# Performance work log

Measured on AMD Instinct MI355X. Metric: run time of the kernel, lower is better.

## Reference

```python
import jax, jax.numpy as jnp
import numpy as np

B = 65536
NUM_INPUTS = 128
H0, H1 = 512, 512
K = 200
MIN_W = 0.001
MIN_H = 0.001
MIN_D = 0.001
EDGE_CONST = float(np.log(np.exp(1.0 - 0.001) - 1.0))  # in-place edge derivative value
LN_EPS = 1e-5


def setup_inputs() -> dict:
    key = jax.random.key(0)
    ks = jax.random.split(key, 10)
    f32 = jnp.float32
    inputs = jax.random.normal(ks[0], (B, NUM_INPUTS), dtype=f32)
    W1 = jax.random.normal(ks[1], (H0, NUM_INPUTS), dtype=f32) / np.sqrt(NUM_INPUTS)
    b1 = jnp.zeros((H0,), f32)
    g1 = jnp.ones((H0,), f32)
    be1 = jnp.zeros((H0,), f32)
    W2 = jax.random.normal(ks[2], (H1, H0), dtype=f32) / np.sqrt(H0)
    b2 = jnp.zeros((H1,), f32)
    g2 = jnp.ones((H1,), f32)
    be2 = jnp.zeros((H1,), f32)
    WV = jax.random.normal(ks[3], (3 * K - 1, H1), dtype=f32) / np.sqrt(H1)
    bV = jnp.zeros((3 * K - 1,), f32)
    Wa = jax.random.normal(ks[4], (1, H1), dtype=f32) / np.sqrt(H1)
    ba = jnp.zeros((1,), f32)
    Wb = jax.random.normal(ks[5], (1, H1), dtype=f32) / np.sqrt(H1)
    bb = jnp.zeros((1,), f32)
    return {"inputs": inputs, "W1": W1, "b1": b1, "g1": g1, "be1": be1,
            "W2": W2, "b2": b2, "g2": g2, "be2": be2,
            "WV": WV, "bV": bV, "Wa": Wa, "ba": ba, "Wb": Wb, "bb": bb}


def _layernorm(x, g, b):
    m = jnp.mean(x, axis=-1, keepdims=True)
    v = jnp.mean(jnp.square(x - m), axis=-1, keepdims=True)
    return (x - m) * jax.lax.rsqrt(v + LN_EPS) * g + b


def _spline_forward(inputs, W1, b1, g1, be1, W2, b2, g2, be2, WV, bV, Wa, ba, Wb, bb):
    x = jax.nn.relu(_layernorm(inputs @ W1.T + b1, g1, be1))
    x = jax.nn.relu(_layernorm(x @ W2.T + b2, g2, be2))
    sp = x @ WV.T + bV                      # [B, 3K-1]
    scale_a = jnp.exp(x @ Wa.T + ba)        # [B, 1]
    scale_b = x @ Wb.T + bb                 # [B, 1]

    Wp = jax.nn.softmax(sp[:, :K], axis=1)
    Hp = jax.nn.softmax(sp[:, K:2 * K], axis=1)
    Dp = sp[:, 2 * K:]                      # [B, K-1]
    Wp = MIN_W + (1.0 - MIN_W * K) * Wp
    Hp = MIN_H + (1.0 - MIN_H * K) * Hp
    Dp = MIN_D + jax.nn.softplus(Dp)
    bsz = inputs.shape[0]
    edge = jnp.full((bsz, 1), EDGE_CONST, dtype=inputs.dtype)
    D = jnp.concatenate([edge, Dp, edge], axis=-1)          # [B, K+1]

    zero = jnp.zeros((bsz, 1), dtype=inputs.dtype)
    cw = jnp.concatenate([zero, jnp.cumsum(Wp, axis=-1)], axis=-1)
    cw = cw.at[:, -1].set(1.0)                              # [B, K+1]
    widths = cw[:, 1:] - cw[:, :-1]                         # [B, K]
    ch = jnp.concatenate([zero, jnp.cumsum(Hp, axis=-1)], axis=-1)
    ch = scale_a * ch + scale_b                             # [B, K+1]
    heights = ch[:, 1:] - ch[:, :-1]                        # [B, K]

    tau = ((jnp.arange(K, dtype=inputs.dtype) + 0.5) / K)   # [K]
    tau = jnp.broadcast_to(tau, (bsz, K))

    # sum(tau >= bins) - 1 == searchsorted(bins, tau, side='right') - 1
    bin_idx = jax.vmap(lambda b, t: jnp.searchsorted(b, t, side='right'))(cw, tau) - 1

    ta = lambda a: jnp.take_along_axis(a, bin_idx, axis=-1)
    in_cw = ta(cw)
    in_w = ta(widths)
    in_ch = ta(ch)
    in_h = ta(heights)
    in_delta = ta(heights / widths)
    d0 = ta(D)
    d1 = ta(D[:, 1:])

    theta = (tau - in_cw) / in_w
    t1mt = theta * (1.0 - theta)
    numer = in_h * (in_delta * jnp.square(theta) + d0 * t1mt)
    denom = in_delta + (d0 + d1 - 2.0 * in_delta) * t1mt
    return in_ch + numer / denom            # [B, K]


def reference(inputs, W1, b1, g1, be1, W2, b2, g2, be2, WV, bV, Wa, ba, Wb, bb):
    return _spline_forward(inputs, W1, b1, g1, be1, W2, b2, g2, be2, WV, bV, Wa, ba, Wb, bb)
```

## Files before the change

kernel.cpp:

```cpp
#include <hip/hip_runtime.h>
#include <stdint.h>

typedef __bf16 bf16;
typedef __bf16 bf16x8 __attribute__((ext_vector_type(8)));
typedef __bf16 bf16x4 __attribute__((ext_vector_type(4)));
typedef float  f32x4  __attribute__((ext_vector_type(4)));
typedef uint32_t u32;

#define BATCH    65536
#define NCAT     640
#define SPSTRIDE 604

__device__ __forceinline__ void async16(const void* g, void* l) {
    __builtin_amdgcn_global_load_lds(
        (const u32 __attribute__((address_space(1)))*)g,
        (u32 __attribute__((address_space(3)))*)l,
        16, 0, 0);
}

__global__ __launch_bounds__(256) void prep_kernel(
    const float* W1, const float* W2, const float* WV,
    const float* bV, const float* Wa, const float* ba,
    const float* Wb, const float* bb,
    bf16* w1b, bf16* w2b, bf16* wcat, float* bcat)
{
    int idx = blockIdx.x * 256 + threadIdx.x;
    const int n1 = 512 * 128, n2 = 512 * 512, n3 = NCAT * 512;
    if (idx < n1) { w1b[idx] = (bf16)W1[idx]; return; }
    idx -= n1;
    if (idx < n2) { w2b[idx] = (bf16)W2[idx]; return; }
    idx -= n2;
    if (idx < n3) {
        int n = idx >> 9, k = idx & 511;
        float v = 0.f;
        if (n < 599)       v = WV[n * 512 + k];
        else if (n == 599) v = Wa[k];
        else if (n == 600) v = Wb[k];
        wcat[idx] = (bf16)v;
        return;
    }
    idx -= n3;
    if (idx < NCAT) {
        float v = 0.f;
        if (idx < 599)       v = bV[idx];
        else if (idx == 599) v = ba[0];
        else if (idx == 600) v = bb[0];
        bcat[idx] = v;
    }
}

template <int KDIM, bool AF32>
__global__ __launch_bounds__(512, 4) void gemm_ln(
    const void* Av, const bf16* __restrict__ W,
    const float* __restrict__ bias, const float* __restrict__ gamma,
    const float* __restrict__ beta, bf16* out)
{
    constexpr int ABUF = AF32 ? 8192 : 4096;
    __shared__ __align__(16) char smem[2 * ABUF + 65536];
    char* Abase = smem;
    char* Bbase = smem + 2 * ABUF;

    const int t = threadIdx.x;
    const int lane = t & 63, wid = t >> 6;
    const int wm = wid >> 2, wn = wid & 3;
    const int l16 = lane & 15, g16 = lane >> 4;
    const long row0 = (long)blockIdx.x * 64;

    constexpr int NT = KDIM / 32;

    f32x4 acc[2][8];
#pragma unroll
    for (int a = 0; a < 2; ++a)
#pragma unroll
        for (int b = 0; b < 8; ++b) acc[a][b] = (f32x4){0.f, 0.f, 0.f, 0.f};

    auto stageA = [&](int kt, int bi) {
        const int k0 = kt * 32;
        if (AF32) {
            int row = wid * 8 + (lane >> 3);
            int colf = ((lane & 7) * 4) ^ (((lane >> 3) & 7) << 2);
            const float* src = (const float*)Av + (row0 + row) * KDIM + k0 + colf;
            async16(src, Abase + bi * ABUF + wid * 1024);
        } else {
            if (wid < 4) {
                int row = wid * 16 + (lane >> 2);
                const bf16* src = (const bf16*)Av + (row0 + row) * (long)KDIM + k0 + (lane & 3) * 8;
                async16(src, Abase + bi * ABUF + wid * 1024);
            }
        }
    };
    auto stageB = [&](int kt, int bi) {
        const int k0 = kt * 32;
#pragma unroll
        for (int c = 0; c < 4; ++c) {
            int call = wid * 4 + c;
            int row = call * 16 + (lane >> 2);
            const bf16* src = W + (long)row * KDIM + k0 + (lane & 3) * 8;
            async16(src, Bbase + bi * 32768 + call * 1024);
        }
    };

    stageA(0, 0); stageB(0, 0);
    __syncthreads();

    for (int kt = 0; kt < NT; ++kt) {
        const int bi = kt & 1;
        if (kt + 1 < NT) { stageA(kt + 1, bi ^ 1); stageB(kt + 1, bi ^ 1); }

        bf16x8 af[2];
        if (AF32) {
            const float* Af = (const float*)(Abase + bi * ABUF);
#pragma unroll
            for (int fm = 0; fm < 2; ++fm) {
                int r = wm * 32 + fm * 16 + l16;
                int m8 = (r & 7) << 2;
                f32x4 v0 = *(const f32x4*)(Af + r * 32 + ((g16 * 8)     ^ m8));
                f32x4 v1 = *(const f32x4*)(Af + r * 32 + ((g16 * 8 + 4) ^ m8));
                bf16x8 h;
                h[0]=(bf16)v0[0]; h[1]=(bf16)v0[1]; h[2]=(bf16)v0[2]; h[3]=(bf16)v0[3];
                h[4]=(bf16)v1[0]; h[5]=(bf16)v1[1]; h[6]=(bf16)v1[2]; h[7]=(bf16)v1[3];
                af[fm] = h;
            }
        } else {
            const bf16* Ab = (const bf16*)(Abase + bi * ABUF);
#pragma unroll
            for (int fm = 0; fm < 2; ++fm)
                af[fm] = *(const bf16x8*)(Ab + (wm * 32 + fm * 16 + l16) * 32 + g16 * 8);
        }
        const bf16* Bb = (const bf16*)(Bbase + bi * 32768);
#pragma unroll
        for (int fn = 0; fn < 8; ++fn) {
            bf16x8 bv = *(const bf16x8*)(Bb + (wn * 128 + fn * 16 + l16) * 32 + g16 * 8);
            acc[0][fn] = __builtin_amdgcn_mfma_f32_16x16x32_bf16(af[0], bv, acc[0][fn], 0, 0, 0);
            acc[1][fn] = __builtin_amdgcn_mfma_f32_16x16x32_bf16(af[1], bv, acc[1][fn], 0, 0, 0);
        }
        __syncthreads();
    }

    float* Psum = (float*)Abase;
    float* Psq  = (float*)(Abase + 1024);
#pragma unroll
    for (int fm = 0; fm < 2; ++fm)
#pragma unroll
        for (int fn = 0; fn < 8; ++fn) {
            float bv = bias[wn * 128 + fn * 16 + l16];
#pragma unroll
            for (int i = 0; i < 4; ++i) acc[fm][fn][i] += bv;
        }
#pragma unroll
    for (int fm = 0; fm < 2; ++fm)
#pragma unroll
        for (int i = 0; i < 4; ++i) {
            float s = 0.f, q = 0.f;
#pragma unroll
            for (int fn = 0; fn < 8; ++fn) { float v = acc[fm][fn][i]; s += v; q += v * v; }
#pragma unroll
            for (int m = 1; m < 16; m <<= 1) { s += __shfl_xor(s, m); q += __shfl_xor(q, m); }
            if (l16 == 0) {
                int lr = wm * 32 + fm * 16 + g16 * 4 + i;
                Psum[lr * 4 + wn] = s; Psq[lr * 4 + wn] = q;
            }
        }
    __syncthreads();
#pragma unroll
    for (int fm = 0; fm < 2; ++fm)
#pragma unroll
        for (int i = 0; i < 4; ++i) {
            int lr = wm * 32 + fm * 16 + g16 * 4 + i;
            float s = Psum[lr * 4 + 0] + Psum[lr * 4 + 1] + Psum[lr * 4 + 2] + Psum[lr * 4 + 3];
            float q = Psq[lr * 4 + 0] + Psq[lr * 4 + 1] + Psq[lr * 4 + 2] + Psq[lr * 4 + 3];
            float mean = s * (1.f / 512.f);
            float var  = q * (1.f / 512.f) - mean * mean;
            float rstd = rsqrtf(var + 1e-5f);
            long grow = row0 + lr;
#pragma unroll
            for (int fn = 0; fn < 8; ++fn) {
                int col = wn * 128 + fn * 16 + l16;
                float o = (acc[fm][fn][i] - mean) * rstd * gamma[col] + beta[col];
                out[grow * 512 + col] = (bf16)fmaxf(o, 0.f);
            }
        }
}

__global__ __launch_bounds__(512, 2) void gemm_cat(
    const bf16* __restrict__ A, const bf16* __restrict__ W,
    const float* __restrict__ bcat, bf16* __restrict__ sp, float* __restrict__ ab)
{
    __shared__ __align__(16) char smem[16384 + 81920];
    char* Abase = smem;
    char* Bbase = smem + 16384;

    const int t = threadIdx.x;
    const int lane = t & 63, wid = t >> 6;
    const int wm = wid >> 2, wn = wid & 3;
    const int l16 = lane & 15, g16 = lane >> 4;
    const long row0 = (long)blockIdx.x * 128;

    f32x4 acc[4][10];
#pragma unroll
    for (int a = 0; a < 4; ++a)
#pragma unroll
        for (int b = 0; b < 10; ++b) acc[a][b] = (f32x4){0.f, 0.f, 0.f, 0.f};

    auto stageA = [&](int kt, int bi) {
        int row = wid * 16 + (lane >> 2);
        const bf16* src = A + (row0 + row) * 512 + kt * 32 + (lane & 3) * 8;
        async16(src, Abase + bi * 8192 + wid * 1024);
    };
    auto stageB = [&](int kt, int bi) {
#pragma unroll
        for (int c = 0; c < 5; ++c) {
            int call = wid * 5 + c;
            int row = call * 16 + (lane >> 2);
            const bf16* src = W + (long)row * 512 + kt * 32 + (lane & 3) * 8;
            async16(src, Bbase + bi * 40960 + call * 1024);
        }
    };

    stageA(0, 0); stageB(0, 0);
    __syncthreads();

    for (int kt = 0; kt < 16; ++kt) {
        const int bi = kt & 1;
        if (kt < 15) { stageA(kt + 1, bi ^ 1); stageB(kt + 1, bi ^ 1); }
        const bf16* Ab = (const bf16*)(Abase + bi * 8192);
        const bf16* Bb = (const bf16*)(Bbase + bi * 40960);
        bf16x8 af[4];
#pragma unroll
        for (int fm = 0; fm < 4; ++fm)
            af[fm] = *(const bf16x8*)(Ab + (wm * 64 + fm * 16 + l16) * 32 + g16 * 8);
#pragma unroll
        for (int fn = 0; fn < 10; ++fn) {
            bf16x8 bv = *(const bf16x8*)(Bb + (wn * 160 + fn * 16 + l16) * 32 + g16 * 8);
#pragma unroll
            for (int fm = 0; fm < 4; ++fm)
                acc[fm][fn] = __builtin_amdgcn_mfma_f32_16x16x32_bf16(af[fm], bv, acc[fm][fn], 0, 0, 0);
        }
        __syncthreads();
    }

#pragma unroll
    for (int fn = 0; fn < 10; ++fn) {
        int col = wn * 160 + fn * 16 + l16;
        float bv = (col <= 600) ? bcat[col] : 0.f;
#pragma unroll
        for (int fm = 0; fm < 4; ++fm)
#pragma unroll
            for (int i = 0; i < 4; ++i) {
                long grow = row0 + wm * 64 + fm * 16 + g16 * 4 + i;
                float v = acc[fm][fn][i] + bv;
                if (col < 599)       sp[grow * SPSTRIDE + col] = (bf16)v;
                else if (col == 599) ab[grow * 2 + 0] = v;
                else if (col == 600) ab[grow * 2 + 1] = v;
            }
    }
}

__global__ __launch_bounds__(256) void spline_kernel(
    const bf16* __restrict__ sp, const float* __restrict__ ab, float* __restrict__ out)
{
    const int t = threadIdx.x;
    const int lane = t & 63, wid = t >> 6;
    const long row = (long)blockIdx.x * 4 + wid;
    const bf16* spr = sp + row * SPSTRIDE;
    const bool act = lane < 50;
    const float EC = 0.53974247f;

    const float sa = __expf(ab[row * 2 + 0]);
    const float sb = ab[row * 2 + 1];

    auto rng = [](float x) -> int {
        int v = (int)ceilf(fmaf(200.f, x, -0.5f));
        return v < 0 ? 0 : (v > 200 ? 200 : v);
    };

    float p0, p1, p2, p3;
    {
        float x0, x1, x2v, x3;
        if (act) {
            bf16x4 v = *(const bf16x4*)&spr[4 * lane];
            x0 = (float)v[0]; x1 = (float)v[1]; x2v = (float)v[2]; x3 = (float)v[3];
        } else { x0 = x1 = x2v = x3 = -1e30f; }
        float m = fmaxf(fmaxf(x0, x1), fmaxf(x2v, x3));
#pragma unroll
        for (int d = 1; d < 64; d <<= 1) m = fmaxf(m, __shfl_xor(m, d));
        float e0 = act ? __expf(x0 - m) : 0.f;
        float e1 = act ? __expf(x1 - m) : 0.f;
        float e2 = act ? __expf(x2v - m) : 0.f;
        float e3 = act ? __expf(x3 - m) : 0.f;
        float s = e0 + e1 + e2 + e3;
#pragma unroll
        for (int d = 1; d < 64; d <<= 1) s += __shfl_xor(s, d);
        float inv = 0.8f / s;
        p0 = act ? fmaf(e0, inv, 0.001f) : 0.f;
        p1 = act ? fmaf(e1, inv, 0.001f) : 0.f;
        p2 = act ? fmaf(e2, inv, 0.001f) : 0.f;
        p3 = act ? fmaf(e3, inv, 0.001f) : 0.f;
    }
    float c0 = p0, c1 = c0 + p1, c2 = c1 + p2, c3 = c2 + p3;
    float run = c3, ts = run;
#pragma unroll
    for (int d = 1; d < 64; d <<= 1) { float u = __shfl_up(ts, d); if (lane >= d) ts += u; }
    float excl  = ts - run;
    float nexcl = __shfl_down(excl, 1);
    float cwl0 = excl, cwl1 = excl + c0, cwl2 = excl + c1, cwl3 = excl + c2;
    float cwr3 = (lane == 49) ? 1.0f : nexcl;

    float hp0, hp1, hp2, hp3;
    {
        float x0, x1, x2v, x3;
        if (act) {
            bf16x4 v = *(const bf16x4*)&spr[200 + 4 * lane];
            x0 = (float)v[0]; x1 = (float)v[1]; x2v = (float)v[2]; x3 = (float)v[3];
        } else { x0 = x1 = x2v = x3 = -1e30f; }
        float m = fmaxf(fmaxf(x0, x1), fmaxf(x2v, x3));
#pragma unroll
        for (int d = 1; d < 64; d <<= 1) m = fmaxf(m, __shfl_xor(m, d));
        float e0 = act ? __expf(x0 - m) : 0.f;
        float e1 = act ? __expf(x1 - m) : 0.f;
        float e2 = act ? __expf(x2v - m) : 0.f;
        float e3 = act ? __expf(x3 - m) : 0.f;
        float s = e0 + e1 + e2 + e3;
#pragma unroll
        for (int d = 1; d < 64; d <<= 1) s += __shfl_xor(s, d);
        float inv = 0.8f / s;
        hp0 = act ? fmaf(e0, inv, 0.001f) : 0.f;
        hp1 = act ? fmaf(e1, inv, 0.001f) : 0.f;
        hp2 = act ? fmaf(e2, inv, 0.001f) : 0.f;
        hp3 = act ? fmaf(e3, inv, 0.001f) : 0.f;
    }
    float hc0 = hp0, hc1 = hc0 + hp1, hc2 = hc1 + hp2, hc3 = hc2 + hp3;
    float hrun = hc3, hts = hrun;
#pragma unroll
    for (int d = 1; d < 64; d <<= 1) { float u = __shfl_up(hts, d); if (lane >= d) hts += u; }
    float hexcl  = hts - hrun;
    float nhexcl = __shfl_down(hexcl, 1);
    float ch0 = fmaf(sa, hexcl, sb);
    float ch1 = fmaf(sa, hexcl + hc0, sb);
    float ch2 = fmaf(sa, hexcl + hc1, sb);
    float ch3 = fmaf(sa, hexcl + hc2, sb);
    float chr3 = fmaf(sa, nhexcl, sb);

    float dv0, dv1, dv2, dv3;
    {
        float x0 = 0.f, x1 = 0.f, x2v = 0.f, x3 = 0.f;
        if (act) {
            bf16x4 v = *(const bf16x4*)&spr[400 + 4 * lane];
            x0 = (float)v[0]; x1 = (float)v[1]; x2v = (float)v[2]; x3 = (float)v[3];
        }
        auto spls = [](float x) {
            return fmaxf(x, 0.f) + __logf(1.f + __expf(-fabsf(x))) + 0.001f;
        };
        dv0 = spls(x0); dv1 = spls(x1); dv2 = spls(x2v); dv3 = spls(x3);
    }
    if (lane == 49) dv3 = EC;
    float dprev = __shfl_up(dv3, 1);
    if (lane == 0) dprev = EC;

    int b0 = rng(cwl0), b1 = rng(cwl1), b2 = rng(cwl2), b3 = rng(cwl3);
    int b4 = (lane == 49) ? 200 : rng(nexcl);

    if (act) {
        float* orow = out + (size_t)row * 200;
        auto emit = [&](int lo, int hi, float wl, float wr_, float hl, float hr,
                        float d0, float d1) {
            float w = wr_ - wl;
            float h = hr - hl;
            float invw = 1.f / w;
            float delta = h * invw;
            float dd2 = d0 + d1 - 2.f * delta;
            for (int jj = lo; jj < hi; ++jj) {
                float tau = ((float)jj + 0.5f) * (1.f / 200.f);
                float th = (tau - wl) * invw;
                float t1 = th * (1.f - th);
                float numer = h * (delta * th * th + d0 * t1);
                float denom = fmaf(dd2, t1, delta);
                orow[jj] = hl + numer / denom;
            }
        };
        emit(b0, b1, cwl0, cwl1, ch0, ch1, dprev, dv0);
        emit(b1, b2, cwl1, cwl2, ch1, ch2, dv0,   dv1);
        emit(b2, b3, cwl2, cwl3, ch2, ch3, dv1,   dv2);
        emit(b3, b4, cwl3, cwr3, ch3, chr3, dv2,  dv3);
    }
}

extern "C" void kernel_launch(void* const* d_in, const int* in_sizes, int n_in,
                              void* d_out, int out_size, void* d_ws, size_t ws_size,
                              hipStream_t stream)
{
    const float* inputs = (const float*)d_in[0];
    const float* W1  = (const float*)d_in[1];
    const float* b1  = (const float*)d_in[2];
    const float* g1  = (const float*)d_in[3];
    const float* be1 = (const float*)d_in[4];
    const float* W2  = (const float*)d_in[5];
    const float* b2  = (const float*)d_in[6];
    const float* g2  = (const float*)d_in[7];
    const float* be2 = (const float*)d_in[8];
    const float* WV  = (const float*)d_in[9];
    const float* bV  = (const float*)d_in[10];
    const float* Wa  = (const float*)d_in[11];
    const float* ba  = (const float*)d_in[12];
    const float* Wb  = (const float*)d_in[13];
    const float* bb  = (const float*)d_in[14];
    float* out = (float*)d_out;

    char* ws = (char*)d_ws;
    bf16*  w1b  = (bf16*) (ws + 0);
    bf16*  w2b  = (bf16*) (ws + 131072);
    bf16*  wcat = (bf16*) (ws + 655360);
    float* bcat = (float*)(ws + 1310720);
    float* ab   = (float*)(ws + 1313280);
    bf16*  x    = (bf16*) (ws + 2097152);
    bf16*  spb  = (bf16*) (ws + 69206016);

    const int preptot = 512 * 128 + 512 * 512 + NCAT * 512 + NCAT;
    prep_kernel<<<(preptot + 255) / 256, 256, 0, stream>>>(
        W1, W2, WV, bV, Wa, ba, Wb, bb, w1b, w2b, wcat, bcat);

    gemm_ln<128, true ><<<BATCH / 64, 512, 0, stream>>>(inputs, w1b, b1, g1, be1, x);
    gemm_ln<512, false><<<BATCH / 64, 512, 0, stream>>>(x,      w2b, b2, g2, be2, x);
    gemm_cat<<<BATCH / 128, 512, 0, stream>>>(x, wcat, bcat, spb, ab);
    spline_kernel<<<BATCH / 4, 256, 0, stream>>>(spb, ab, out);
}
```

Before: 263.5 us.

## Pre-convert inputs to bf16, split gemm_cat along N, use LDS-indexed spline evaluation

Three separate changes. The prep kernel now converts the fp32 inputs to bf16 up front, so the first GEMM loads bf16 A tiles instead of converting fp32 in LDS. gemm_cat splits its N dimension across two blocks, halving per-block LDS and accumulators so that four blocks can be resident per CU. The spline kernel writes per-row knot tables and a bin index per output into LDS, then has each lane evaluate outputs j = lane + 50k, giving coalesced stores and balanced work instead of variable-length per-lane loops. The extra conversion pass costs one more read and write of the input, and the split GEMM reads the A tile twice.

```diff
diff --git a/kernel.cpp b/kernel.cpp
--- a/kernel.cpp
+++ b/kernel.cpp
@@ -21,11 +21,22 @@
 __global__ __launch_bounds__(256) void prep_kernel(
     const float* W1, const float* W2, const float* WV,
     const float* bV, const float* Wa, const float* ba,
-    const float* Wb, const float* bb,
-    bf16* w1b, bf16* w2b, bf16* wcat, float* bcat)
+    const float* Wb, const float* bb, const float* inputs,
+    bf16* w1b, bf16* w2b, bf16* wcat, float* bcat, bf16* xin)
 {
     int idx = blockIdx.x * 256 + threadIdx.x;
     const int n1 = 512 * 128, n2 = 512 * 512, n3 = NCAT * 512;
+    const int n5 = BATCH * 128 / 8;
+    if (idx < n5) {
+        const float4* src = (const float4*)(inputs + idx * 8);
+        float4 v0 = src[0], v1 = src[1];
+        bf16x8 h;
+        h[0]=(bf16)v0.x; h[1]=(bf16)v0.y; h[2]=(bf16)v0.z; h[3]=(bf16)v0.w;
+        h[4]=(bf16)v1.x; h[5]=(bf16)v1.y; h[6]=(bf16)v1.z; h[7]=(bf16)v1.w;
+        *(bf16x8*)&xin[idx * 8] = h;
+        return;
+    }
+    idx -= n5;
     if (idx < n1) { w1b[idx] = (bf16)W1[idx]; return; }
     idx -= n1;
     if (idx < n2) { w2b[idx] = (bf16)W2[idx]; return; }
@@ -49,23 +60,21 @@
     }
 }
 
-template <int KDIM, bool AF32>
+template <int KDIM>
 __global__ __launch_bounds__(512, 4) void gemm_ln(
-    const void* Av, const bf16* __restrict__ W,
+    const bf16* __restrict__ A, const bf16* __restrict__ W,
     const float* __restrict__ bias, const float* __restrict__ gamma,
     const float* __restrict__ beta, bf16* out)
 {
-    constexpr int ABUF = AF32 ? 8192 : 4096;
-    __shared__ __align__(16) char smem[2 * ABUF + 65536];
+    __shared__ __align__(16) char smem[8192 + 65536];
     char* Abase = smem;
-    char* Bbase = smem + 2 * ABUF;
+    char* Bbase = smem + 8192;
 
     const int t = threadIdx.x;
     const int lane = t & 63, wid = t >> 6;
     const int wm = wid >> 2, wn = wid & 3;
     const int l16 = lane & 15, g16 = lane >> 4;
     const long row0 = (long)blockIdx.x * 64;
-
     constexpr int NT = KDIM / 32;
 
     f32x4 acc[2][8];
@@ -75,27 +84,18 @@
         for (int b = 0; b < 8; ++b) acc[a][b] = (f32x4){0.f, 0.f, 0.f, 0.f};
 
     auto stageA = [&](int kt, int bi) {
-        const int k0 = kt * 32;
-        if (AF32) {
-            int row = wid * 8 + (lane >> 3);
-            int colf = ((lane & 7) * 4) ^ (((lane >> 3) & 7) << 2);
-            const float* src = (const float*)Av + (row0 + row) * KDIM + k0 + colf;
-            async16(src, Abase + bi * ABUF + wid * 1024);
-        } else {
-            if (wid < 4) {
-                int row = wid * 16 + (lane >> 2);
-                const bf16* src = (const bf16*)Av + (row0 + row) * (long)KDIM + k0 + (lane & 3) * 8;
-                async16(src, Abase + bi * ABUF + wid * 1024);
-            }
+        if (wid < 4) {
+            int row = wid * 16 + (lane >> 2);
+            const bf16* src = A + (row0 + row) * (long)KDIM + kt * 32 + (lane & 3) * 8;
+            async16(src, Abase + bi * 4096 + wid * 1024);
         }
     };
     auto stageB = [&](int kt, int bi) {
-        const int k0 = kt * 32;
 #pragma unroll
         for (int c = 0; c < 4; ++c) {
             int call = wid * 4 + c;
             int row = call * 16 + (lane >> 2);
-            const bf16* src = W + (long)row * KDIM + k0 + (lane & 3) * 8;
+            const bf16* src = W + (long)row * KDIM + kt * 32 + (lane & 3) * 8;
             async16(src, Bbase + bi * 32768 + call * 1024);
         }
     };
@@ -106,28 +106,12 @@
     for (int kt = 0; kt < NT; ++kt) {
         const int bi = kt & 1;
         if (kt + 1 < NT) { stageA(kt + 1, bi ^ 1); stageB(kt + 1, bi ^ 1); }
-
+        const bf16* Ab = (const bf16*)(Abase + bi * 4096);
+        const bf16* Bb = (const bf16*)(Bbase + bi * 32768);
         bf16x8 af[2];
-        if (AF32) {
-            const float* Af = (const float*)(Abase + bi * ABUF);
-#pragma unroll
-            for (int fm = 0; fm < 2; ++fm) {
-                int r = wm * 32 + fm * 16 + l16;
-                int m8 = (r & 7) << 2;
-                f32x4 v0 = *(const f32x4*)(Af + r * 32 + ((g16 * 8)     ^ m8));
-                f32x4 v1 = *(const f32x4*)(Af + r * 32 + ((g16 * 8 + 4) ^ m8));
-                bf16x8 h;
-                h[0]=(bf16)v0[0]; h[1]=(bf16)v0[1]; h[2]=(bf16)v0[2]; h[3]=(bf16)v0[3];
-                h[4]=(bf16)v1[0]; h[5]=(bf16)v1[1]; h[6]=(bf16)v1[2]; h[7]=(bf16)v1[3];
-                af[fm] = h;
-            }
-        } else {
-            const bf16* Ab = (const bf16*)(Abase + bi * ABUF);
-#pragma unroll
-            for (int fm = 0; fm < 2; ++fm)
-                af[fm] = *(const bf16x8*)(Ab + (wm * 32 + fm * 16 + l16) * 32 + g16 * 8);
-        }
-        const bf16* Bb = (const bf16*)(Bbase + bi * 32768);
+#pragma unroll
+        for (int fm = 0; fm < 2; ++fm)
+            af[fm] = *(const bf16x8*)(Ab + (wm * 32 + fm * 16 + l16) * 32 + g16 * 8);
 #pragma unroll
         for (int fn = 0; fn < 8; ++fn) {
             bf16x8 bv = *(const bf16x8*)(Bb + (wn * 128 + fn * 16 + l16) * 32 + g16 * 8);
@@ -182,11 +166,11 @@
         }
 }
 
-__global__ __launch_bounds__(512, 2) void gemm_cat(
+__global__ __launch_bounds__(512, 4) void gemm_cat(
     const bf16* __restrict__ A, const bf16* __restrict__ W,
     const float* __restrict__ bcat, bf16* __restrict__ sp, float* __restrict__ ab)
 {
-    __shared__ __align__(16) char smem[16384 + 81920];
+    __shared__ __align__(16) char smem[16384 + 40960];
     char* Abase = smem;
     char* Bbase = smem + 16384;
 
@@ -194,13 +178,14 @@
     const int lane = t & 63, wid = t >> 6;
     const int wm = wid >> 2, wn = wid & 3;
     const int l16 = lane & 15, g16 = lane >> 4;
-    const long row0 = (long)blockIdx.x * 128;
-
-    f32x4 acc[4][10];
+    const int nh  = blockIdx.x & 1;
+    const long row0 = (long)(blockIdx.x >> 1) * 128;
+
+    f32x4 acc[4][5];
 #pragma unroll
     for (int a = 0; a < 4; ++a)
 #pragma unroll
-        for (int b = 0; b < 10; ++b) acc[a][b] = (f32x4){0.f, 0.f, 0.f, 0.f};
+        for (int b = 0; b < 5; ++b) acc[a][b] = (f32x4){0.f, 0.f, 0.f, 0.f};
 
     auto stageA = [&](int kt, int bi) {
         int row = wid * 16 + (lane >> 2);
@@ -209,11 +194,13 @@
     };
     auto stageB = [&](int kt, int bi) {
 #pragma unroll
-        for (int c = 0; c < 5; ++c) {
-            int call = wid * 5 + c;
-            int row = call * 16 + (lane >> 2);
-            const bf16* src = W + (long)row * 512 + kt * 32 + (lane & 3) * 8;
-            async16(src, Bbase + bi * 40960 + call * 1024);
+        for (int c = 0; c < 3; ++c) {
+            int call = c * 8 + wid;
+            if (call < 20) {
+                int row = nh * 320 + call * 16 + (lane >> 2);
+                const bf16* src = W + (long)row * 512 + kt * 32 + (lane & 3) * 8;
+                async16(src, Bbase + bi * 20480 + call * 1024);
+            }
         }
     };
 
@@ -224,14 +211,14 @@
         const int bi = kt & 1;
         if (kt < 15) { stageA(kt + 1, bi ^ 1); stageB(kt + 1, bi ^ 1); }
         const bf16* Ab = (const bf16*)(Abase + bi * 8192);
-        const bf16* Bb = (const bf16*)(Bbase + bi * 40960);
+        const bf16* Bb = (const bf16*)(Bbase + bi * 20480);
         bf16x8 af[4];
 #pragma unroll
         for (int fm = 0; fm < 4; ++fm)
             af[fm] = *(const bf16x8*)(Ab + (wm * 64 + fm * 16 + l16) * 32 + g16 * 8);
 #pragma unroll
-        for (int fn = 0; fn < 10; ++fn) {
-            bf16x8 bv = *(const bf16x8*)(Bb + (wn * 160 + fn * 16 + l16) * 32 + g16 * 8);
+        for (int fn = 0; fn < 5; ++fn) {
+            bf16x8 bv = *(const bf16x8*)(Bb + (wn * 80 + fn * 16 + l16) * 32 + g16 * 8);
 #pragma unroll
             for (int fm = 0; fm < 4; ++fm)
                 acc[fm][fn] = __builtin_amdgcn_mfma_f32_16x16x32_bf16(af[fm], bv, acc[fm][fn], 0, 0, 0);
@@ -240,8 +227,8 @@
     }
 
 #pragma unroll
-    for (int fn = 0; fn < 10; ++fn) {
-        int col = wn * 160 + fn * 16 + l16;
+    for (int fn = 0; fn < 5; ++fn) {
+        int col = nh * 320 + wn * 80 + fn * 16 + l16;
         float bv = (col <= 600) ? bcat[col] : 0.f;
 #pragma unroll
         for (int fm = 0; fm < 4; ++fm)
@@ -259,12 +246,17 @@
 __global__ __launch_bounds__(256) void spline_kernel(
     const bf16* __restrict__ sp, const float* __restrict__ ab, float* __restrict__ out)
 {
+    __shared__ float S[4][816];
     const int t = threadIdx.x;
     const int lane = t & 63, wid = t >> 6;
     const long row = (long)blockIdx.x * 4 + wid;
     const bf16* spr = sp + row * SPSTRIDE;
     const bool act = lane < 50;
     const float EC = 0.53974247f;
+    float* cw = &S[wid][0];
+    float* ch = &S[wid][204];
+    float* dd = &S[wid][408];
+    int*   bx = (int*)&S[wid][612];
 
     const float sa = __expf(ab[row * 2 + 0]);
     const float sb = ab[row * 2 + 1];
@@ -304,7 +296,6 @@
     float excl  = ts - run;
     float nexcl = __shfl_down(excl, 1);
     float cwl0 = excl, cwl1 = excl + c0, cwl2 = excl + c1, cwl3 = excl + c2;
-    float cwr3 = (lane == 49) ? 1.0f : nexcl;
 
     float hp0, hp1, hp2, hp3;
     {
@@ -333,13 +324,11 @@
     float hrun = hc3, hts = hrun;
 #pragma unroll
     for (int d = 1; d < 64; d <<= 1) { float u = __shfl_up(hts, d); if (lane >= d) hts += u; }
-    float hexcl  = hts - hrun;
-    float nhexcl = __shfl_down(hexcl, 1);
+    float hexcl = hts - hrun;
     float ch0 = fmaf(sa, hexcl, sb);
     float ch1 = fmaf(sa, hexcl + hc0, sb);
     float ch2 = fmaf(sa, hexcl + hc1, sb);
     float ch3 = fmaf(sa, hexcl + hc2, sb);
-    float chr3 = fmaf(sa, nhexcl, sb);
 
     float dv0, dv1, dv2, dv3;
     {
@@ -357,31 +346,46 @@
     float dprev = __shfl_up(dv3, 1);
     if (lane == 0) dprev = EC;
 
-    int b0 = rng(cwl0), b1 = rng(cwl1), b2 = rng(cwl2), b3 = rng(cwl3);
-    int b4 = (lane == 49) ? 200 : rng(nexcl);
+    if (act) {
+        *(f32x4*)&cw[4 * lane] = (f32x4){cwl0, cwl1, cwl2, cwl3};
+        *(f32x4*)&ch[4 * lane] = (f32x4){ch0, ch1, ch2, ch3};
+        *(f32x4*)&dd[4 * lane] = (f32x4){dprev, dv0, dv1, dv2};
+    }
+    if (lane == 49) {
+        cw[200] = 1.0f;
+        ch[200] = fmaf(sa, hts, sb);
+        dd[200] = EC;
+    }
+
+    if (act) {
+        int b0 = rng(cwl0), b1 = rng(cwl1), b2 = rng(cwl2), b3 = rng(cwl3);
+        int b4 = (lane == 49) ? 200 : rng(nexcl);
+        for (int j = b0; j < b1; ++j) bx[j] = 4 * lane;
+        for (int j = b1; j < b2; ++j) bx[j] = 4 * lane + 1;
+        for (int j = b2; j < b3; ++j) bx[j] = 4 * lane + 2;
+        for (int j = b3; j < b4; ++j) bx[j] = 4 * lane + 3;
+    }
+    asm volatile("s_waitcnt lgkmcnt(0)" ::: "memory");
 
     if (act) {
         float* orow = out + (size_t)row * 200;
-        auto emit = [&](int lo, int hi, float wl, float wr_, float hl, float hr,
-                        float d0, float d1) {
-            float w = wr_ - wl;
-            float h = hr - hl;
+#pragma unroll
+        for (int k = 0; k < 4; ++k) {
+            int j = lane + 50 * k;
+            int b = bx[j];
+            float wl = cw[b], wr = cw[b + 1];
+            float hl = ch[b], hr = ch[b + 1];
+            float d0 = dd[b], d1 = dd[b + 1];
+            float tau = ((float)j + 0.5f) * (1.f / 200.f);
+            float w = wr - wl, h = hr - hl;
             float invw = 1.f / w;
             float delta = h * invw;
-            float dd2 = d0 + d1 - 2.f * delta;
-            for (int jj = lo; jj < hi; ++jj) {
-                float tau = ((float)jj + 0.5f) * (1.f / 200.f);
-                float th = (tau - wl) * invw;
-                float t1 = th * (1.f - th);
-                float numer = h * (delta * th * th + d0 * t1);
-                float denom = fmaf(dd2, t1, delta);
-                orow[jj] = hl + numer / denom;
-            }
-        };
-        emit(b0, b1, cwl0, cwl1, ch0, ch1, dprev, dv0);
-        emit(b1, b2, cwl1, cwl2, ch1, ch2, dv0,   dv1);
-        emit(b2, b3, cwl2, cwl3, ch2, ch3, dv1,   dv2);
-        emit(b3, b4, cwl3, cwr3, ch3, chr3, dv2,  dv3);
+            float th = (tau - wl) * invw;
+            float t1 = th * (1.f - th);
+            float numer = h * fmaf(delta * th, th, d0 * t1);
+            float denom = fmaf(d0 + d1 - 2.f * delta, t1, delta);
+            orow[j] = hl + numer / denom;
+        }
     }
 }
 
@@ -414,13 +418,14 @@
     float* ab   = (float*)(ws + 1313280);
     bf16*  x    = (bf16*) (ws + 2097152);
     bf16*  spb  = (bf16*) (ws + 69206016);
-
-    const int preptot = 512 * 128 + 512 * 512 + NCAT * 512 + NCAT;
+    bf16*  xin  = (bf16*) (ws + 69206016);
+
+    const int preptot = BATCH * 128 / 8 + 512 * 128 + 512 * 512 + NCAT * 512 + NCAT;
     prep_kernel<<<(preptot + 255) / 256, 256, 0, stream>>>(
-        W1, W2, WV, bV, Wa, ba, Wb, bb, w1b, w2b, wcat, bcat);
-
-    gemm_ln<128, true ><<<BATCH / 64, 512, 0, stream>>>(inputs, w1b, b1, g1, be1, x);
-    gemm_ln<512, false><<<BATCH / 64, 512, 0, stream>>>(x,      w2b, b2, g2, be2, x);
-    gemm_cat<<<BATCH / 128, 512, 0, stream>>>(x, wcat, bcat, spb, ab);
+        W1, W2, WV, bV, Wa, ba, Wb, bb, inputs, w1b, w2b, wcat, bcat, xin);
+
+    gemm_ln<128><<<BATCH / 64, 512, 0, stream>>>(xin, w1b, b1, g1, be1, x);
+    gemm_ln<512><<<BATCH / 64, 512, 0, stream>>>(x,   w2b, b2, g2, be2, x);
+    gemm_cat<<<(BATCH / 128) * 2, 512, 0, stream>>>(x, wcat, bcat, spb, ab);
     spline_kernel<<<BATCH / 4, 256, 0, stream>>>(spb, ab, out);
 }
```

Result: no change. 258.5 us (-1.9%).
